# Kernel optimization log

Hardware: AMD Instinct MI355X
Metric: run time of the kernel (lower is better)

## Reference

```python
import jax, jax.numpy as jnp
import numpy as np
from jax import lax

# Orthonormal 2x2 Haar (db1). Analysis uses dwt_scale per coefficient; the
# synthesis uses 0.5*idwt_scale so that dwt_scale=0.5, idwt_scale=1.0 gives a
# perfect round trip (Hadamard matrix M, M@M = 4I, M symmetric).
DWT_SCALE = 0.5
IDWT_SCALE = 1.0
WT_LEVELS = 3
STRIDE = 1
PAD = 1  # (kernel_size - 1) // 2


def dwt2(x, s):
    # x: (B, C, H, W) -> (B, C, 4, H/2, W/2), subband order LL, LH, HL, HH
    a = x[..., 0::2, 0::2]
    b = x[..., 0::2, 1::2]
    c = x[..., 1::2, 0::2]
    d = x[..., 1::2, 1::2]
    ll = (a + b + c + d) * s
    lh = (a - b + c - d) * s
    hl = (a + b - c - d) * s
    hh = (a - b - c + d) * s
    return jnp.stack([ll, lh, hl, hh], axis=2)


def idwt2(sub, s):
    # sub: (B, C, 4, h, w) -> (B, C, 2h, 2w); inverse of dwt2 when s = 0.5/ (4*dwt_s) * ... here Hadamard symmetric
    ll, lh, hl, hh = sub[:, :, 0], sub[:, :, 1], sub[:, :, 2], sub[:, :, 3]
    a = (ll + lh + hl + hh) * s
    b = (ll - lh + hl - hh) * s
    c = (ll + lh - hl - hh) * s
    d = (ll - lh - hl + hh) * s
    B, C, h, w = a.shape
    row0 = jnp.stack([a, b], axis=-1).reshape(B, C, h, 2 * w)
    row1 = jnp.stack([c, d], axis=-1).reshape(B, C, h, 2 * w)
    return jnp.stack([row0, row1], axis=-2).reshape(B, C, 2 * h, 2 * w)


def conv2d(x, w, stride, pad):
    return lax.conv_general_dilated(
        x, w, window_strides=(stride, stride),
        padding=[(pad, pad), (pad, pad)],
        dimension_numbers=('NCHW', 'OIHW', 'NCHW'))


def wtconv_core(x, weight):
    cout4 = weight.shape[0]
    cout = cout4 // 4
    curr_ll = x
    ll_levels, high_levels = [], []
    for _ in range(WT_LEVELS):
        sub = dwt2(curr_ll, DWT_SCALE)             # (B, C, 4, h, w)
        B, C, _, h, w = sub.shape
        y = conv2d(sub.reshape(B, C * 4, h, w), weight, STRIDE, PAD)
        y = y.reshape(B, cout, 4, h, w)
        ll_levels.append(y[:, :, 0])
        high_levels.append(y[:, :, 1:])
        curr_ll = sub[:, :, 0]                     # pre-conv LL feeds next level
    next_ll = jnp.zeros_like(ll_levels[-1])
    for ll, hi in zip(reversed(ll_levels), reversed(high_levels)):
        ll = ll + next_ll
        sub = jnp.concatenate([ll[:, :, None], hi], axis=2)
        next_ll = idwt2(sub, 0.5 * IDWT_SCALE)
    return next_ll


def setup_inputs() -> dict:
    key = jax.random.key(0)
    k1, k2, k3 = jax.random.split(key, 3)
    B, C, H, W = 8, 32, 224, 224
    K = 3
    x = jax.random.normal(k1, (B, C, H, W), dtype=jnp.float32)
    fan_in = C * 4 * K * K
    bound = np.sqrt(6.0 / ((1.0 + 2.236 ** 2) * fan_in))
    weight = jax.random.uniform(k2, (C * 4, C * 4, K, K), dtype=jnp.float32,
                                minval=-bound, maxval=bound)
    bias = jax.random.normal(k3, (C,), dtype=jnp.float32) * 0.01
    return {"x": x, "weight": weight, "bias": bias}


def reference(x, weight, bias):
    H, W = x.shape[-2:]
    pad_factor = 2 ** WT_LEVELS
    pad_h = (pad_factor - H % pad_factor) % pad_factor
    pad_w = (pad_factor - W % pad_factor) % pad_factor
    xp = x
    if pad_h > 0 or pad_w > 0:
        xp = jnp.pad(x, ((0, 0), (0, 0), (0, pad_h), (0, pad_w)), mode='reflect')
    out = wtconv_core(xp, weight)
    out = out[..., :H, :W]
    return out + bias[None, :, None, None]
```

## Files before the change

kernel.cpp:

```cpp
#include <hip/hip_runtime.h>

typedef __bf16 bf16_t;
typedef __bf16 bf16x4_t __attribute__((ext_vector_type(4)));
typedef __bf16 bf16x8_t __attribute__((ext_vector_type(8)));
typedef float f32x16_t __attribute__((ext_vector_type(16)));

#define AS_G(p) ((const __attribute__((address_space(1))) void*)(p))
#define AS_L(p) ((__attribute__((address_space(3))) void*)(p))
#define DRAIN_VM() asm volatile("s_waitcnt vmcnt(0)" ::: "memory")

__device__ __forceinline__ void repack_body(const float* __restrict__ w,
                                            bf16_t* __restrict__ wt2,
                                            int o) {
  int e = o & 7;
  int lane = (o >> 3) & 63;
  int f = o >> 9;
  int wc = f & 1;
  int nt = (f >> 1) & 1;
  int kc = (f >> 2) & 3;
  int hk = (f >> 4) & 1;
  int t = f >> 5;
  int oc = wc * 64 + nt * 32 + (lane & 31);
  int ic = (hk * 8 + kc * 2 + (lane >> 5)) * 8 + e;
  wt2[o] = (bf16_t)w[((size_t)oc * 128 + ic) * 9 + t];
}

__device__ __forceinline__ void dwt_body(const float* __restrict__ in,
                                         bf16_t* __restrict__ sub,
                                         float* __restrict__ llout,
                                         int h, int w, int bi, int i, int j0,
                                         bf16_t* lds) {
  const int tid = threadIdx.x;
  const int j = tid & 63;
  const int cg = tid >> 6;
  const int jg = j0 + j;
  const bool jok = jg < w;
  const int H2 = h * 2, W2 = w * 2;
  for (int c = cg; c < 32; c += 4) {
    float va = 0.f, vb = 0.f, vc = 0.f, vd = 0.f;
    if (jok) {
      const float2* p0 = (const float2*)(in + ((size_t)(bi * 32 + c) * H2 + 2 * i) * W2);
      const float2* p1 = (const float2*)(in + ((size_t)(bi * 32 + c) * H2 + 2 * i + 1) * W2);
      float2 r0 = p0[jg];
      float2 r1 = p1[jg];
      va = r0.x; vb = r0.y; vc = r1.x; vd = r1.y;
    }
    float ll = (va + vb + vc + vd) * 0.5f;
    float lh = (va - vb + vc - vd) * 0.5f;
    float hl = (va + vb - vc - vd) * 0.5f;
    float hh = (va - vb - vc + vd) * 0.5f;
    bf16x4_t q;
    q.x = (bf16_t)ll; q.y = (bf16_t)lh; q.z = (bf16_t)hl; q.w = (bf16_t)hh;
    *(bf16x4_t*)(&lds[j * 132 + c * 4]) = q;
    if (llout != nullptr && jok)
      llout[((size_t)(bi * 32 + c) * h + i) * w + jg] = ll;
  }
  __syncthreads();
  const size_t obase = ((size_t)bi * h + i) * w;
  for (int it = 0; it < 8; ++it) {
    int flat = it * 256 + tid;
    int jj = flat >> 5;
    int c4 = flat & 31;
    if (j0 + jj < w) {
      bf16x4_t q = *(const bf16x4_t*)(&lds[jj * 132 + c4 * 4]);
      *(bf16x4_t*)(sub + ((obase + j0 + jj) << 7) + c4 * 4) = q;
    }
  }
}

__global__ __launch_bounds__(256) void dwt1x_kernel(const float* __restrict__ x,
                                                    bf16_t* __restrict__ sub1,
                                                    float* __restrict__ ll1,
                                                    const float* __restrict__ wsrc,
                                                    bf16_t* __restrict__ wt2) {
  __shared__ __align__(16) bf16_t lds[64 * 132];
  if (blockIdx.z == 8) {
    int bid = blockIdx.y;
    for (int o = bid * 256 + threadIdx.x; o < 147456; o += 56 * 256)
      repack_body(wsrc, wt2, o);
    return;
  }
  const int bi = blockIdx.z;
  const int i = blockIdx.y;
  const int tid = threadIdx.x;
  const int j = tid & 63;
  const int cg = tid >> 6;
  const int h = 56, w = 56;
  const bool jok = j < w;
  for (int c = cg; c < 32; c += 4) {
    float va = 0.f, vb = 0.f, vc = 0.f, vd = 0.f;
    if (jok) {
      const float* base = x + ((size_t)(bi * 32 + c) * 224 + 4 * i) * 224;
      float4 p0 = ((const float4*)(base))[j];
      float4 p1 = ((const float4*)(base + 224))[j];
      float4 p2 = ((const float4*)(base + 448))[j];
      float4 p3 = ((const float4*)(base + 672))[j];
      va = (p0.x + p0.y + p1.x + p1.y) * 0.5f;
      vb = (p0.z + p0.w + p1.z + p1.w) * 0.5f;
      vc = (p2.x + p2.y + p3.x + p3.y) * 0.5f;
      vd = (p2.z + p2.w + p3.z + p3.w) * 0.5f;
    }
    float ll = (va + vb + vc + vd) * 0.5f;
    float lh = (va - vb + vc - vd) * 0.5f;
    float hl = (va + vb - vc - vd) * 0.5f;
    float hh = (va - vb - vc + vd) * 0.5f;
    bf16x4_t q;
    q.x = (bf16_t)ll; q.y = (bf16_t)lh; q.z = (bf16_t)hl; q.w = (bf16_t)hh;
    *(bf16x4_t*)(&lds[j * 132 + c * 4]) = q;
    if (jok)
      ll1[((size_t)(bi * 32 + c) * h + i) * w + j] = ll;
  }
  __syncthreads();
  const size_t obase = ((size_t)bi * h + i) * w;
  for (int it = 0; it < 8; ++it) {
    int flat = it * 256 + tid;
    int jj = flat >> 5;
    int c4 = flat & 31;
    if (jj < w) {
      bf16x4_t q = *(const bf16x4_t*)(&lds[jj * 132 + c4 * 4]);
      *(bf16x4_t*)(sub1 + ((obase + jj) << 7) + c4 * 4) = q;
    }
  }
}

__global__ __launch_bounds__(256) void dwt_kernel(const float* __restrict__ in,
                                                  bf16_t* __restrict__ sub,
                                                  float* __restrict__ llout,
                                                  int h, int w) {
  __shared__ __align__(16) bf16_t lds[64 * 132];
  dwt_body(in, sub, llout, h, w, blockIdx.z, blockIdx.y, blockIdx.x * 64, lds);
}

__device__ __forceinline__ void conv_idwt_tile(
    const bf16_t* __restrict__ sub, const bf16_t* __restrict__ wt2,
    const float* __restrict__ nll, const float* __restrict__ nllup,
    const float* __restrict__ bias, float* __restrict__ out,
    int h, int w, int bi, int y0, int x0, int och, uint4* smemV) {
  char* haloS = (char*)smemV;
  char* Bbuf = (char*)smemV + 23040;
  float* scr = (float*)((char*)smemV + 23040);
  const int tid = threadIdx.x;
  const size_t img_base = (size_t)bi * h * w;

  const int lane = tid & 63;
  const int wv = tid >> 6;
  const int m = lane & 31;
  const int hw_ = lane >> 5;
  const int il = wv * 2 + (m >> 4);
  const int jl = m & 15;
  const int pixA = il * 18 + jl;

  f32x16_t acc[2] = {};

  for (int hk = 0; hk < 2; ++hk) {
    if (hk) __syncthreads();
    for (int it = 0; it < 6; ++it) {
      int flat = it * 256 + tid;
      int pix = flat >> 3;
      int ch = flat & 7;
      if (pix < 180) {
        int r = pix / 18;
        int c = pix - r * 18;
        int gy = y0 + r - 1;
        int gx = x0 + c - 1;
        uint4 v = make_uint4(0u, 0u, 0u, 0u);
        if ((unsigned)gy < (unsigned)h && (unsigned)gx < (unsigned)w)
          v = *(const uint4*)(sub + ((img_base + (size_t)gy * w + gx) << 7) +
                              ((hk * 8 + ch) << 3));
        *(uint4*)(haloS + (pix << 7) + ((ch ^ (pix & 7)) << 4)) = v;
      }
    }
    {
      const int th0 = hk;
#pragma unroll
      for (int q = 0; q < 2; ++q) {
        const bf16_t* srcp = wt2 + (((th0 << 4) + (wv << 2) + (q << 1) + och) << 9) + (lane << 3);
        __builtin_amdgcn_global_load_lds(AS_G(srcp),
            AS_L(Bbuf + (((wv << 1) + q) << 10)), 16, 0, 0);
      }
    }
    DRAIN_VM();
    __syncthreads();

    int cur = 0;
    for (int t = 0; t < 9; ++t) {
      if (t < 8) {
        const int thn = ((t + 1) << 1) + hk;
#pragma unroll
        for (int q = 0; q < 2; ++q) {
          const bf16_t* srcp = wt2 + (((thn << 4) + (wv << 2) + (q << 1) + och) << 9) + (lane << 3);
          __builtin_amdgcn_global_load_lds(AS_G(srcp),
              AS_L(Bbuf + ((cur ^ 1) << 13) + (((wv << 1) + q) << 10)), 16, 0, 0);
        }
      }
      const int ky = t / 3;
      const int kx = t - ky * 3;
      const int pix0 = pixA + ky * 18 + kx;
      const int s0 = pix0 & 7;
      const char* hp0 = haloS + (pix0 << 7);
      const char* bp = Bbuf + (cur << 13) + (lane << 4);
#pragma unroll
      for (int kc = 0; kc < 4; ++kc) {
        bf16x8_t b0 = *(const bf16x8_t*)(bp + ((kc << 1) << 10));
        bf16x8_t b1 = *(const bf16x8_t*)(bp + (((kc << 1) + 1) << 10));
        const int cidx = kc * 2 + hw_;
        bf16x8_t a0 = *(const bf16x8_t*)(hp0 + ((cidx ^ s0) << 4));
        acc[0] = __builtin_amdgcn_mfma_f32_32x32x16_bf16(a0, b0, acc[0], 0, 0, 0);
        acc[1] = __builtin_amdgcn_mfma_f32_32x32x16_bf16(a0, b1, acc[1], 0, 0, 0);
      }
      DRAIN_VM();
      __syncthreads();
      cur ^= 1;
    }
  }

  const int W2 = w * 2;
  const int H2 = h * 2;
  const int hu = h >> 1, wu = w >> 1;
  const int mh_t = m >> 4;
  const int mm = m & 15;
  const int kw = mm >> 2;
  const int sw = mm & 3;

#pragma unroll
  for (int ph = 0; ph < 4; ++ph) {
    const int nt = ph >> 1;
    const int mh = ph & 1;
    if (ph) __syncthreads();
    if (mh_t == mh) {
#pragma unroll
      for (int reg = 0; reg < 16; ++reg) {
        int row = (reg & 3) + ((reg >> 2) << 3) + (hw_ << 2);
        int px = wv * 32 + row;
        scr[px * 17 + (kw << 2) + sw] = acc[nt][reg];
      }
    }
    __syncthreads();
#pragma unroll
    for (int it = 0; it < 2; ++it) {
      int idx = it * 256 + tid;
      int ox4 = idx & 7;
      int dy = (idx >> 3) & 1;
      int row = (idx >> 4) & 7;
      int k = (idx >> 7) & 3;
      int gy = y0 + row;
      int gx = x0 + ox4 * 2;
      if (gy >= h || gx >= w) continue;
      int p0 = row * 16 + ox4 * 2;
      int p1 = p0 + 1;
      float4 sa = *(const float4*)(&scr[p0 * 17 + (k << 2)]);
      float4 sb = *(const float4*)(&scr[p1 * 17 + (k << 2)]);
      float sg = dy ? -1.f : 1.f;
      float e0 = sa.x + sa.y + sg * (sa.z + sa.w);
      float e1 = sa.x - sa.y + sg * (sa.z - sa.w);
      float e2 = sb.x + sb.y + sg * (sb.z + sb.w);
      float e3 = sb.x - sb.y + sg * (sb.z - sb.w);
      int ch = och * 16 + nt * 8 + mh * 4 + k;
      float n0 = 0.f, n1 = 0.f;
      if (nll != nullptr) {
        const float* np = nll + ((size_t)(bi * 32 + ch) * h + gy) * w + gx;
        float2 nv = *(const float2*)np;
        n0 = nv.x; n1 = nv.y;
      }
      if (nllup != nullptr) {
        float u = nllup[((size_t)(bi * 32 + ch) * hu + (gy >> 1)) * wu + (gx >> 1)];
        n0 += 0.5f * u;
        n1 += 0.5f * u;
      }
      float bv = (bias != nullptr) ? bias[ch] : 0.f;
      float4 o;
      o.x = 0.5f * e0 + 0.5f * n0 + bv;
      o.y = 0.5f * e1 + 0.5f * n0 + bv;
      o.z = 0.5f * e2 + 0.5f * n1 + bv;
      o.w = 0.5f * e3 + 0.5f * n1 + bv;
      float* op = out + ((size_t)(bi * 32 + ch) * H2 + 2 * gy + dy) * W2 + 2 * gx;
      *(float4*)op = o;
    }
  }
}

__global__ __launch_bounds__(256, 4) void conv_idwt_kernel(
    const bf16_t* __restrict__ sub, const bf16_t* __restrict__ wt2,
    const float* __restrict__ nll, const float* __restrict__ nllup,
    const float* __restrict__ bias, float* __restrict__ out, int h, int w) {
  __shared__ uint4 smemV[2464];
  conv_idwt_tile(sub, wt2, nll, nllup, bias, out, h, w,
                 blockIdx.z, blockIdx.y * 8, (blockIdx.x >> 1) * 16,
                 blockIdx.x & 1, smemV);
}

__global__ __launch_bounds__(256, 4) void conv12s_kernel(
    const float* __restrict__ x, bf16_t* __restrict__ sub0,
    const bf16_t* __restrict__ sub1, const bf16_t* __restrict__ sub2,
    const bf16_t* __restrict__ wt2, float* __restrict__ nll1raw,
    float* __restrict__ nll2) {
  __shared__ uint4 smemV[2464];
  const int B = blockIdx.x;
  if (B >= 576) {
    int r = B - 576;
    int bx = r & 1;
    int rr = r >> 1;
    int i = rr % 112;
    int bi = rr / 112;
    dwt_body(x, sub0, nullptr, 112, 112, bi, i, bx * 64, (bf16_t*)smemV);
    return;
  }
  const bf16_t* sub;
  float* outp;
  int hh, bi, by, bx, och;
  if (B < 448) {
    och = B & 1;
    int q = B >> 1;
    bx = q & 3;
    int r = q >> 2;
    by = r % 7;
    bi = r / 7;
    sub = sub1; outp = nll1raw; hh = 56;
  } else {
    int lb = B - 448;
    och = lb & 1;
    int q = lb >> 1;
    bx = q & 1;
    int r = q >> 1;
    by = r & 3;
    bi = r >> 2;
    sub = sub2; outp = nll2; hh = 28;
  }
  conv_idwt_tile(sub, wt2, nullptr, nullptr, nullptr, outp, hh, hh,
                 bi, by * 8, bx * 16, och, smemV);
}

extern "C" void kernel_launch(void* const* d_in, const int* in_sizes, int n_in,
                              void* d_out, int out_size, void* d_ws, size_t ws_size,
                              hipStream_t stream) {
  if (ws_size < 66125824u) return;

  const float* x = (const float*)d_in[0];
  const float* weight = (const float*)d_in[1];
  const float* bias = (const float*)d_in[2];
  float* out = (float*)d_out;
  char* ws = (char*)d_ws;

  bf16_t* wt2 = (bf16_t*)(ws);
  bf16_t* sub0 = (bf16_t*)(ws + 294912);
  bf16_t* sub1 = (bf16_t*)(ws + 25985024);
  bf16_t* sub2 = (bf16_t*)(ws + 32407552);
  float* ll1 = (float*)(ws + 46858240);
  float* nll2 = (float*)(ws + 50069504);
  float* nll1 = (float*)(ws + 53280768);

  dwt1x_kernel<<<dim3(1, 56, 9), 256, 0, stream>>>(x, sub1, ll1, weight, wt2);
  dwt_kernel<<<dim3(1, 28, 8), 256, 0, stream>>>(ll1, sub2, nullptr, 28, 28);
  conv12s_kernel<<<2368, 256, 0, stream>>>(x, sub0, sub1, sub2, wt2, nll1, nll2);
  conv_idwt_kernel<<<dim3(14, 14, 8), 256, 0, stream>>>(sub0, wt2, nll1, nll2, bias, out, 112, 112);
}
```

Baseline: 177.9 us.

## Merge all three level convolutions into one launch and add a residual fixup pass

```diff
diff --git a/kernel.cpp b/kernel.cpp
--- a/kernel.cpp
+++ b/kernel.cpp
@@ -68,21 +68,30 @@
   }
 }
 
-__global__ __launch_bounds__(256) void dwt1x_kernel(const float* __restrict__ x,
-                                                    bf16_t* __restrict__ sub1,
-                                                    float* __restrict__ ll1,
-                                                    const float* __restrict__ wsrc,
-                                                    bf16_t* __restrict__ wt2) {
+__global__ __launch_bounds__(256) void stage1_kernel(
+    const float* __restrict__ x, bf16_t* __restrict__ sub0,
+    bf16_t* __restrict__ sub1, float* __restrict__ ll1,
+    const float* __restrict__ wsrc, bf16_t* __restrict__ wt2) {
   __shared__ __align__(16) bf16_t lds[64 * 132];
-  if (blockIdx.z == 8) {
-    int bid = blockIdx.y;
-    for (int o = bid * 256 + threadIdx.x; o < 147456; o += 56 * 256)
+  const int B = blockIdx.x;
+  const int tid = threadIdx.x;
+  if (B >= 2240) {
+    int bid = B - 2240;
+    for (int o = bid * 256 + tid; o < 147456; o += 56 * 256)
       repack_body(wsrc, wt2, o);
     return;
   }
-  const int bi = blockIdx.z;
-  const int i = blockIdx.y;
-  const int tid = threadIdx.x;
+  if (B >= 448) {
+    int r = B - 448;
+    int bx = r & 1;
+    int rr = r >> 1;
+    int i = rr % 112;
+    int bi = rr / 112;
+    dwt_body(x, sub0, nullptr, 112, 112, bi, i, bx * 64, lds);
+    return;
+  }
+  const int bi = B / 56;
+  const int i = B % 56;
   const int j = tid & 63;
   const int cg = tid >> 6;
   const int h = 56, w = 56;
@@ -133,9 +142,8 @@
 
 __device__ __forceinline__ void conv_idwt_tile(
     const bf16_t* __restrict__ sub, const bf16_t* __restrict__ wt2,
-    const float* __restrict__ nll, const float* __restrict__ nllup,
-    const float* __restrict__ bias, float* __restrict__ out,
-    int h, int w, int bi, int y0, int x0, int och, uint4* smemV) {
+    float* __restrict__ out, int h, int w, int bi, int y0, int x0, int och,
+    uint4* smemV) {
   char* haloS = (char*)smemV;
   char* Bbuf = (char*)smemV + 23040;
   float* scr = (float*)((char*)smemV + 23040);
@@ -216,7 +224,6 @@
 
   const int W2 = w * 2;
   const int H2 = h * 2;
-  const int hu = h >> 1, wu = w >> 1;
   const int mh_t = m >> 4;
   const int mm = m & 15;
   const int kw = mm >> 2;
@@ -256,78 +263,72 @@
       float e2 = sb.x + sb.y + sg * (sb.z + sb.w);
       float e3 = sb.x - sb.y + sg * (sb.z - sb.w);
       int ch = och * 16 + nt * 8 + mh * 4 + k;
-      float n0 = 0.f, n1 = 0.f;
-      if (nll != nullptr) {
-        const float* np = nll + ((size_t)(bi * 32 + ch) * h + gy) * w + gx;
-        float2 nv = *(const float2*)np;
-        n0 = nv.x; n1 = nv.y;
-      }
-      if (nllup != nullptr) {
-        float u = nllup[((size_t)(bi * 32 + ch) * hu + (gy >> 1)) * wu + (gx >> 1)];
-        n0 += 0.5f * u;
-        n1 += 0.5f * u;
-      }
-      float bv = (bias != nullptr) ? bias[ch] : 0.f;
+      float* op = out + ((size_t)(bi * 32 + ch) * H2 + 2 * gy + dy) * W2 + 2 * gx;
       float4 o;
-      o.x = 0.5f * e0 + 0.5f * n0 + bv;
-      o.y = 0.5f * e1 + 0.5f * n0 + bv;
-      o.z = 0.5f * e2 + 0.5f * n1 + bv;
-      o.w = 0.5f * e3 + 0.5f * n1 + bv;
-      float* op = out + ((size_t)(bi * 32 + ch) * H2 + 2 * gy + dy) * W2 + 2 * gx;
+      o.x = 0.5f * e0; o.y = 0.5f * e1; o.z = 0.5f * e2; o.w = 0.5f * e3;
       *(float4*)op = o;
     }
   }
 }
 
-__global__ __launch_bounds__(256, 4) void conv_idwt_kernel(
-    const bf16_t* __restrict__ sub, const bf16_t* __restrict__ wt2,
-    const float* __restrict__ nll, const float* __restrict__ nllup,
-    const float* __restrict__ bias, float* __restrict__ out, int h, int w) {
-  __shared__ uint4 smemV[2464];
-  conv_idwt_tile(sub, wt2, nll, nllup, bias, out, h, w,
-                 blockIdx.z, blockIdx.y * 8, (blockIdx.x >> 1) * 16,
-                 blockIdx.x & 1, smemV);
-}
-
-__global__ __launch_bounds__(256, 4) void conv12s_kernel(
-    const float* __restrict__ x, bf16_t* __restrict__ sub0,
-    const bf16_t* __restrict__ sub1, const bf16_t* __restrict__ sub2,
-    const bf16_t* __restrict__ wt2, float* __restrict__ nll1raw,
+__global__ __launch_bounds__(256, 4) void megaconv_kernel(
+    const bf16_t* __restrict__ sub0, const bf16_t* __restrict__ sub1,
+    const bf16_t* __restrict__ sub2, const bf16_t* __restrict__ wt2,
+    float* __restrict__ out, float* __restrict__ nll1raw,
     float* __restrict__ nll2) {
   __shared__ uint4 smemV[2464];
   const int B = blockIdx.x;
-  if (B >= 576) {
-    int r = B - 576;
-    int bx = r & 1;
-    int rr = r >> 1;
-    int i = rr % 112;
-    int bi = rr / 112;
-    dwt_body(x, sub0, nullptr, 112, 112, bi, i, bx * 64, (bf16_t*)smemV);
+  if (B < 1568) {
+    int xx = B % 14;
+    int rem = B / 14;
+    int yy = rem % 14;
+    int bi = rem / 14;
+    conv_idwt_tile(sub0, wt2, out, 112, 112, bi, yy * 8, (xx >> 1) * 16,
+                   xx & 1, smemV);
     return;
   }
-  const bf16_t* sub;
-  float* outp;
-  int hh, bi, by, bx, och;
-  if (B < 448) {
-    och = B & 1;
-    int q = B >> 1;
-    bx = q & 3;
+  if (B < 2016) {
+    int lb = B - 1568;
+    int och = lb & 1;
+    int q = lb >> 1;
+    int bx = q & 3;
     int r = q >> 2;
-    by = r % 7;
-    bi = r / 7;
-    sub = sub1; outp = nll1raw; hh = 56;
-  } else {
-    int lb = B - 448;
-    och = lb & 1;
+    int by = r % 7;
+    int bi = r / 7;
+    conv_idwt_tile(sub1, wt2, nll1raw, 56, 56, bi, by * 8, bx * 16, och, smemV);
+    return;
+  }
+  {
+    int lb = B - 2016;
+    int och = lb & 1;
     int q = lb >> 1;
-    bx = q & 1;
+    int bx = q & 1;
     int r = q >> 1;
-    by = r & 3;
-    bi = r >> 2;
-    sub = sub2; outp = nll2; hh = 28;
-  }
-  conv_idwt_tile(sub, wt2, nullptr, nullptr, nullptr, outp, hh, hh,
-                 bi, by * 8, bx * 16, och, smemV);
+    int by = r & 3;
+    int bi = r >> 2;
+    conv_idwt_tile(sub2, wt2, nll2, 28, 28, bi, by * 8, bx * 16, och, smemV);
+  }
+}
+
+__global__ __launch_bounds__(256) void fixup_kernel(
+    float* __restrict__ out, const float* __restrict__ nll1,
+    const float* __restrict__ nll2, const float* __restrict__ bias) {
+  int g = blockIdx.x * 256 + threadIdx.x;
+  int q = g % 56;
+  int r1 = g / 56;
+  int oy = r1 % 224;
+  int r2 = r1 / 224;
+  int c = r2 & 31;
+  int b = r2 >> 5;
+  float2 n1 = *(const float2*)(nll1 + ((size_t)(b * 32 + c) * 112 + (oy >> 1)) * 112 + 2 * q);
+  float n2 = nll2[((size_t)(b * 32 + c) * 56 + (oy >> 2)) * 56 + q];
+  float bv = bias[c];
+  float add0 = 0.5f * n1.x + 0.25f * n2 + bv;
+  float add1 = 0.5f * n1.y + 0.25f * n2 + bv;
+  float* op = out + ((size_t)(b * 32 + c) * 224 + oy) * 224 + 4 * q;
+  float4 v = *(float4*)op;
+  v.x += add0; v.y += add0; v.z += add1; v.w += add1;
+  *(float4*)op = v;
 }
 
 extern "C" void kernel_launch(void* const* d_in, const int* in_sizes, int n_in,
@@ -349,8 +350,8 @@
   float* nll2 = (float*)(ws + 50069504);
   float* nll1 = (float*)(ws + 53280768);
 
-  dwt1x_kernel<<<dim3(1, 56, 9), 256, 0, stream>>>(x, sub1, ll1, weight, wt2);
+  stage1_kernel<<<2296, 256, 0, stream>>>(x, sub0, sub1, ll1, weight, wt2);
   dwt_kernel<<<dim3(1, 28, 8), 256, 0, stream>>>(ll1, sub2, nullptr, 28, 28);
-  conv12s_kernel<<<2368, 256, 0, stream>>>(x, sub0, sub1, sub2, wt2, nll1, nll2);
-  conv_idwt_kernel<<<dim3(14, 14, 8), 256, 0, stream>>>(sub0, wt2, nll1, nll2, bias, out, 112, 112);
-}
+  megaconv_kernel<<<2144, 256, 0, stream>>>(sub0, sub1, sub2, wt2, out, nll1, nll2);
+  fixup_kernel<<<12544, 256, 0, stream>>>(out, nll1, nll2, bias);
+}
```

After: 190.6 us. 7.1% more time.
